# Performance work log

Measured on AMD Instinct MI355X. Metric: run time of the kernel, lower is better.

The kernel has to match this reference:

```python
import jax, jax.numpy as jnp
import numpy as np

D_MODEL = 1024
NUM_HEADS = 16
D_K = D_MODEL // NUM_HEADS


def setup_inputs() -> dict:
    key = jax.random.key(0)
    ks = jax.random.split(key, 11)
    B, S = 2, 2048
    s = 1.0 / np.sqrt(D_MODEL)
    return {
        "q": jax.random.normal(ks[0], (B, S, D_MODEL), jnp.float32),
        "k": jax.random.normal(ks[1], (B, S, D_MODEL), jnp.float32),
        "v": jax.random.normal(ks[2], (B, S, D_MODEL), jnp.float32),
        "w_q": jax.random.normal(ks[3], (D_MODEL, D_MODEL), jnp.float32) * s,
        "b_q": jnp.zeros((D_MODEL,), jnp.float32),
        "w_k": jax.random.normal(ks[4], (D_MODEL, D_MODEL), jnp.float32) * s,
        "b_k": jnp.zeros((D_MODEL,), jnp.float32),
        "w_v": jax.random.normal(ks[5], (D_MODEL, D_MODEL), jnp.float32) * s,
        "b_v": jnp.zeros((D_MODEL,), jnp.float32),
        "w_o": jax.random.normal(ks[6], (D_MODEL, D_MODEL), jnp.float32) * s,
        "b_o": jnp.zeros((D_MODEL,), jnp.float32),
    }


def reference(q, k, v, w_q, b_q, w_k, b_k, w_v, b_v, w_o, b_o):
    B, S, _ = q.shape
    H, Dk = NUM_HEADS, D_K

    def split_heads(x):  # [B,S,D] -> [B,H,S,Dk]
        return x.reshape(B, S, H, Dk).transpose(0, 2, 1, 3)

    # torch nn.Linear: x @ W.T + b
    qh = split_heads(q @ w_q.T + b_q)
    kh = split_heads(k @ w_k.T + b_k)
    vh = split_heads(v @ w_v.T + b_v)

    scale = 1.0 / jnp.sqrt(jnp.asarray(Dk, qh.dtype))
    scores = jnp.einsum("bhsd,bhtd->bhst", qh, kh) * scale  # [B,H,S,S]
    attn = jax.nn.softmax(scores, axis=-1)
    # dropout is identity in eval/deterministic baseline
    out = jnp.einsum("bhst,bhtd->bhsd", attn, vh)  # [B,H,S,Dk]
    out = out.transpose(0, 2, 1, 3).reshape(B, S, H * Dk)
    return out @ w_o.T + b_o
```

## Files before the change

### kernel.cpp

```cpp
#include <hip/hip_runtime.h>
#include <hip/hip_bf16.h>
#include <stdint.h>

typedef unsigned short u16;
typedef __attribute__((ext_vector_type(8))) short short8;
typedef __attribute__((ext_vector_type(8))) __bf16 bf16x8;
typedef __attribute__((ext_vector_type(4))) float f32x4;
typedef __attribute__((ext_vector_type(4))) uint32_t u32x4;

#if defined(__has_builtin)
#if __has_builtin(__builtin_amdgcn_global_load_lds)
#define USE_GLLDS 1
#endif
#endif

#if defined(__has_builtin)
#if __has_builtin(__builtin_amdgcn_exp2f)
#define HAVE_EXP2_BUILTIN 1
#endif
#endif
__device__ __forceinline__ float fexp2(float x) {
#ifdef HAVE_EXP2_BUILTIN
  return __builtin_amdgcn_exp2f(x);
#else
  return exp2f(x);
#endif
}

__device__ __forceinline__ u16 f2bf(float f) {
  __hip_bfloat16 h = __float2bfloat16(f);
  return __builtin_bit_cast(u16, h);
}

__device__ __forceinline__ uint32_t cvt_pk_bf16(float lo, float hi) {
  uint32_t w;
  asm("v_cvt_pk_bf16_f32 %0, %1, %2" : "=v"(w) : "v"(lo), "v"(hi));
  return w;
}

__device__ __forceinline__ f32x4 mfma16(bf16x8 a, bf16x8 b, f32x4 c) {
  return __builtin_amdgcn_mfma_f32_16x16x32_bf16(a, b, c, 0, 0, 0);
}

#ifdef USE_GLLDS
__device__ __forceinline__ void async_cp16(const void* g, void* l) {
  __builtin_amdgcn_global_load_lds(
      (const __attribute__((address_space(1))) void*)g,
      (__attribute__((address_space(3))) void*)l, 16, 0, 0);
}
#endif

__global__ __launch_bounds__(256) void cvt_all(
    const float* __restrict__ q, const float* __restrict__ k,
    const float* __restrict__ v, const float* __restrict__ w0,
    const float* __restrict__ w1, const float* __restrict__ w2,
    const float* __restrict__ w3, u16* __restrict__ dst) {
  size_t i = ((size_t)blockIdx.x * 256 + threadIdx.x) * 8;
  const size_t M1 = 1u << 20;
  const float* s;
  size_t base;
  if (i < 4 * M1) { s = q; base = 0; }
  else if (i < 8 * M1) { s = k; base = 4 * M1; }
  else if (i < 12 * M1) { s = v; base = 8 * M1; }
  else if (i < 13 * M1) { s = w0; base = 12 * M1; }
  else if (i < 14 * M1) { s = w1; base = 13 * M1; }
  else if (i < 15 * M1) { s = w2; base = 14 * M1; }
  else { s = w3; base = 15 * M1; }
  const float4 a = *(const float4*)(s + (i - base));
  const float4 b = *(const float4*)(s + (i - base) + 4);
  short8 r;
  r[0] = (short)f2bf(a.x); r[1] = (short)f2bf(a.y);
  r[2] = (short)f2bf(a.z); r[3] = (short)f2bf(a.w);
  r[4] = (short)f2bf(b.x); r[5] = (short)f2bf(b.y);
  r[6] = (short)f2bf(b.z); r[7] = (short)f2bf(b.w);
  *(short8*)(dst + i) = r;
}

__device__ __forceinline__ void gemm_core8(const u16* __restrict__ X,
                                           const u16* __restrict__ W,
                                           const float* __restrict__ bias,
                                           void* __restrict__ outp, int mode,
                                           int m0, int n0) {
  __shared__ u16 Al[128 * 64];
  __shared__ u16 Bl[128 * 64];
  const int tid = threadIdx.x;
  const int wv = tid >> 6, l = tid & 63;
  const int wr = wv >> 2, wc = wv & 3;
  const int lrow = l & 15, g = l >> 4;
  const int rswe = (lrow & 7) << 3;

  f32x4 acc[4][2];
#pragma unroll
  for (int i = 0; i < 4; ++i)
#pragma unroll
    for (int j = 0; j < 2; ++j) acc[i][j] = (f32x4){0.f, 0.f, 0.f, 0.f};

  const int srow = l >> 3;
  const int gcol = ((l & 7) ^ srow) * 8;
  const u16* Asrc = X + (size_t)(m0 + wv * 8 + srow) * 1024 + gcol;
  const u16* Bsrc = W + (size_t)(wv * 8 + srow) * 1024 + gcol;

  for (int kt = 0; kt < 1024; kt += 64) {
#ifdef USE_GLLDS
    async_cp16(Asrc + kt, &Al[(wv * 8) * 64]);
    async_cp16(Asrc + (size_t)64 * 1024 + kt, &Al[(wv * 8 + 64) * 64]);
    async_cp16(Bsrc + kt, &Bl[(wv * 8) * 64]);
    async_cp16(Bsrc + (size_t)64 * 1024 + kt, &Bl[(wv * 8 + 64) * 64]);
#else
    short8 a0 = *(const short8*)(Asrc + kt);
    short8 a1 = *(const short8*)(Asrc + (size_t)64 * 1024 + kt);
    short8 b0 = *(const short8*)(Bsrc + kt);
    short8 b1 = *(const short8*)(Bsrc + (size_t)64 * 1024 + kt);
    *(short8*)&Al[(wv * 8 + srow) * 64 + (l & 7) * 8] = a0;
    *(short8*)&Al[(wv * 8 + 64 + srow) * 64 + (l & 7) * 8] = a1;
    *(short8*)&Bl[(wv * 8 + srow) * 64 + (l & 7) * 8] = b0;
    *(short8*)&Bl[(wv * 8 + 64 + srow) * 64 + (l & 7) * 8] = b1;
#endif
    __syncthreads();
#pragma unroll
    for (int ks = 0; ks < 2; ++ks) {
      bf16x8 af[4], bf[2];
      const int qoff = (((ks * 4 + g) << 3) ^ rswe);
#pragma unroll
      for (int mf = 0; mf < 4; ++mf)
        af[mf] = *(const bf16x8*)&Al[(wr * 64 + mf * 16 + lrow) * 64 + qoff];
#pragma unroll
      for (int nf = 0; nf < 2; ++nf)
        bf[nf] = *(const bf16x8*)&Bl[(wc * 32 + nf * 16 + lrow) * 64 + qoff];
#pragma unroll
      for (int mf = 0; mf < 4; ++mf)
#pragma unroll
        for (int nf = 0; nf < 2; ++nf)
          acc[mf][nf] = mfma16(af[mf], bf[nf], acc[mf][nf]);
    }
    __syncthreads();
  }

  const int rb = (l >> 4) * 4;
#pragma unroll
  for (int mf = 0; mf < 4; ++mf) {
#pragma unroll
    for (int nf = 0; nf < 2; ++nf) {
      const int gn = n0 + wc * 32 + nf * 16 + lrow;
      const float bi = bias[gn];
#pragma unroll
      for (int r = 0; r < 4; ++r) {
        const int gm = m0 + wr * 64 + mf * 16 + rb + r;
        float val = acc[mf][nf][r] + bi;
        const int b = gm >> 11, s = gm & 2047, h = gn >> 6, d = gn & 63;
        if (mode == 3) {
          ((float*)outp)[(size_t)gm * 1024 + gn] = val;
        } else if (mode == 2) {
          ((u16*)outp)[(((size_t)((b * 16 + h) * 64 + d)) << 11) + s] = f2bf(val);
        } else {
          if (mode == 0) val *= 0.18033688f;
          ((u16*)outp)[(((size_t)((b * 16 + h) * 2048 + s)) << 6) + d] = f2bf(val);
        }
      }
    }
  }
}

__global__ __launch_bounds__(512, 6) void gemm_proj(
    const u16* __restrict__ qb, const u16* __restrict__ wqb,
    const float* __restrict__ b_q, const float* __restrict__ b_k,
    const float* __restrict__ b_v, u16* __restrict__ Qh) {
  const int s = blockIdx.x;
  const int xcd = s & 7, c = s >> 3;
  const int nx = (xcd >> 2) * 12 + (c % 12);
  const int my = (xcd & 3) * 8 + (c / 12);
  const int z = nx >> 3, nxl = nx & 7;
  const float* bias = (z == 0) ? b_q : ((z == 1) ? b_k : b_v);
  gemm_core8(qb + ((size_t)z << 22), wqb + ((size_t)nx << 17), bias,
             Qh + ((size_t)z << 22), z, my * 128, nxl * 128);
}

__global__ __launch_bounds__(512, 6) void gemm_out(
    const u16* __restrict__ X, const u16* __restrict__ W,
    const float* __restrict__ bias, float* __restrict__ out) {
  const int s = blockIdx.x;
  const int xcd = s & 7, c = s >> 3;
  const int nx = (xcd >> 2) * 4 + (c & 3);
  const int my = (xcd & 3) * 8 + (c >> 2);
  gemm_core8(X, W + ((size_t)nx << 17), bias, out, 3, my * 128, nx * 128);
}

__global__ __launch_bounds__(512, 4) void flash_attn7(
    const u16* __restrict__ Qh, const u16* __restrict__ Kh,
    const u16* __restrict__ VT, u16* __restrict__ Op,
    float2* __restrict__ ml) {
  __shared__ __align__(16) u16 Kbuf[2][4096];
  __shared__ __align__(16) u16 Vbuf[2][4096];
  __shared__ __align__(16) uint32_t Pl[8 * 576];

  const int tid = threadIdx.x;
  const int wv = tid >> 6, l = tid & 63;
  const int q = l & 15, g = l >> 4;

  const int s_lin = blockIdx.x + (blockIdx.y << 4) + (blockIdx.z << 9);
  const int o = ((s_lin & 7) << 7) + (s_lin >> 3);
  const int qt = o & 15, bh = (o >> 4) & 31, z = o >> 9;

  const u16* Qp = Qh + ((size_t)bh * 2048 + qt * 128 + wv * 16) * 64;
  const u16* Kp = Kh + (size_t)bh * 2048 * 64;
  const u16* Vp = VT + (size_t)bh * 64 * 2048;

  bf16x8 qf[2];
  qf[0] = *(const bf16x8*)(Qp + q * 64 + g * 8);
  qf[1] = *(const bf16x8*)(Qp + q * 64 + 32 + g * 8);

  f32x4 o_acc[4];
#pragma unroll
  for (int df = 0; df < 4; ++df) o_acc[df] = (f32x4){0.f, 0.f, 0.f, 0.f};
  float m = -1e30f, ls = 0.f;

  const int srow = l >> 3;
  const int scolq = (l & 7) ^ srow;
  const int pbase = wv * 576 + q * 36;
  const char* kb0 = (const char*)&Kbuf[0][0];
  const char* kb1 = (const char*)&Kbuf[1][0];
  const char* vb0 = (const char*)&Vbuf[0][0];
  const char* vb1 = (const char*)&Vbuf[1][0];
  const int rsw = (q & 7) << 4;

  const u16* kg = Kp + (size_t)(z * 1024 + wv * 8 + srow) * 64 + scolq * 8;
  const u16* vg = Vp + (size_t)(wv * 8 + srow) * 2048 + z * 1024 + scolq * 8;

  {
    short8 k0 = *(const short8*)kg;
    short8 k1 = *(const short8*)(kg + 4096);
    short8 v0 = *(const short8*)vg;
    short8 v1 = *(const short8*)(vg + 64);
    *(short8*)&Kbuf[0][wv * 512 + l * 8] = k0;
    *(short8*)&Kbuf[1][wv * 512 + l * 8] = k1;
    *(short8*)&Vbuf[0][wv * 512 + l * 8] = v0;
    *(short8*)&Vbuf[1][wv * 512 + l * 8] = v1;
  }
  kg += 8192;
  vg += 128;
  __syncthreads();

  for (int tt = 0; tt < 8; ++tt) {
    short8 kr0, kr1, vr0, vr1;
    if (tt < 7) {
      kr0 = *(const short8*)kg;
      kr1 = *(const short8*)(kg + 4096);
      vr0 = *(const short8*)vg;
      vr1 = *(const short8*)(vg + 64);
      kg += 8192;
      vg += 128;
    }

    f32x4 s0[4], s1[4];
#pragma unroll
    for (int nj = 0; nj < 4; ++nj) {
      s0[nj] = (f32x4){0.f, 0.f, 0.f, 0.f};
      s1[nj] = (f32x4){0.f, 0.f, 0.f, 0.f};
    }
#pragma unroll
    for (int ks = 0; ks < 2; ++ks) {
#pragma unroll
      for (int nj = 0; nj < 4; ++nj) {
        const int off = (nj * 16 + q) * 128 + (((ks * 4 + g) << 4) ^ rsw);
        bf16x8 kf0 = *(const bf16x8*)(kb0 + off);
        bf16x8 kf1 = *(const bf16x8*)(kb1 + off);
        s0[nj] = mfma16(kf0, qf[ks], s0[nj]);
        s1[nj] = mfma16(kf1, qf[ks], s1[nj]);
      }
    }

    float mt = s0[0][0];
#pragma unroll
    for (int nj = 0; nj < 4; ++nj)
#pragma unroll
      for (int r = 0; r < 4; ++r) {
        mt = fmaxf(mt, s0[nj][r]);
        mt = fmaxf(mt, s1[nj][r]);
      }
    mt = fmaxf(mt, __shfl_xor(mt, 16));
    mt = fmaxf(mt, __shfl_xor(mt, 32));
    if (!__all(mt <= m + 8.f)) {
      const float nm = fmaxf(m, mt);
      const float rf = fexp2(m - nm);
      m = nm;
      ls *= rf;
#pragma unroll
      for (int df = 0; df < 4; ++df) o_acc[df] *= rf;
    }
    float ps = 0.f;
#pragma unroll
    for (int nj = 0; nj < 4; ++nj)
#pragma unroll
      for (int r = 0; r < 4; ++r) {
        s0[nj][r] = fexp2(s0[nj][r] - m);
        s1[nj][r] = fexp2(s1[nj][r] - m);
        ps += s0[nj][r] + s1[nj][r];
      }
    ps += __shfl_xor(ps, 16);
    ps += __shfl_xor(ps, 32);
    ls += ps;

#pragma unroll
    for (int nj = 0; nj < 4; ++nj)
#pragma unroll
      for (int pp = 0; pp < 2; ++pp)
        Pl[pbase + nj * 8 + g * 2 + pp] =
            cvt_pk_bf16(s0[nj][2 * pp], s0[nj][2 * pp + 1]);
#pragma unroll
    for (int ks = 0; ks < 2; ++ks) {
      u32x4 pw = *(const u32x4*)&Pl[pbase + ks * 16 + 4 * g];
      bf16x8 pf = __builtin_bit_cast(bf16x8, pw);
#pragma unroll
      for (int df = 0; df < 4; ++df) {
        bf16x8 vf = *(const bf16x8*)(vb0 + (df * 16 + q) * 128 +
                                     (((ks * 4 + g) << 4) ^ rsw));
        o_acc[df] = mfma16(vf, pf, o_acc[df]);
      }
    }

#pragma unroll
    for (int nj = 0; nj < 4; ++nj)
#pragma unroll
      for (int pp = 0; pp < 2; ++pp)
        Pl[pbase + nj * 8 + g * 2 + pp] =
            cvt_pk_bf16(s1[nj][2 * pp], s1[nj][2 * pp + 1]);
#pragma unroll
    for (int ks = 0; ks < 2; ++ks) {
      u32x4 pw = *(const u32x4*)&Pl[pbase + ks * 16 + 4 * g];
      bf16x8 pf = __builtin_bit_cast(bf16x8, pw);
#pragma unroll
      for (int df = 0; df < 4; ++df) {
        bf16x8 vf = *(const bf16x8*)(vb1 + (df * 16 + q) * 128 +
                                     (((ks * 4 + g) << 4) ^ rsw));
        o_acc[df] = mfma16(vf, pf, o_acc[df]);
      }
    }

    __syncthreads();
    if (tt < 7) {
      *(short8*)&Kbuf[0][wv * 512 + l * 8] = kr0;
      *(short8*)&Kbuf[1][wv * 512 + l * 8] = kr1;
      *(short8*)&Vbuf[0][wv * 512 + l * 8] = vr0;
      *(short8*)&Vbuf[1][wv * 512 + l * 8] = vr1;
    }
    __syncthreads();
  }

  const float inv = 1.f / ls;
  const int rowb = qt * 128 + wv * 16 + q;
  const size_t prow = (size_t)(z * 32 + bh) * 2048 + rowb;
  u16* Po = Op + (prow << 6);
#pragma unroll
  for (int df = 0; df < 4; ++df)
#pragma unroll
    for (int pp = 0; pp < 2; ++pp) {
      uint32_t w = cvt_pk_bf16(o_acc[df][2 * pp] * inv,
                               o_acc[df][2 * pp + 1] * inv);
      *(uint32_t*)(Po + df * 16 + 4 * g + 2 * pp) = w;
    }
  if (g == 0) ml[prow] = make_float2(m, ls);
}

__global__ __launch_bounds__(256) void combine(
    const uint32_t* __restrict__ Op32, const float2* __restrict__ ml,
    u16* __restrict__ AO) {
  const int j = blockIdx.x * 256 + threadIdx.x;
  const int rowid = j >> 5, w5 = j & 31;
  const float2 a = ml[rowid];
  const float2 c = ml[(1 << 16) + rowid];
  const float M = fmaxf(a.x, c.x);
  float w1 = a.y * fexp2(a.x - M);
  float w2 = c.y * fexp2(c.x - M);
  const float inv = 1.f / (w1 + w2);
  w1 *= inv;
  w2 *= inv;
  const uint32_t p1 = Op32[j];
  const uint32_t p2 = Op32[(1u << 21) + j];
  const float lo = w1 * __builtin_bit_cast(float, p1 << 16) +
                   w2 * __builtin_bit_cast(float, p2 << 16);
  const float hi = w1 * __builtin_bit_cast(float, p1 & 0xffff0000u) +
                   w2 * __builtin_bit_cast(float, p2 & 0xffff0000u);
  const uint32_t outw = cvt_pk_bf16(lo, hi);
  const int bh = rowid >> 11, s = rowid & 2047, b = bh >> 4, h = bh & 15;
  ((uint32_t*)AO)[((size_t)(b * 2048 + s) << 9) + h * 32 + w5] = outw;
}

extern "C" void kernel_launch(void* const* d_in, const int* in_sizes, int n_in,
                              void* d_out, int out_size, void* d_ws,
                              size_t ws_size, hipStream_t stream) {
  const float* q = (const float*)d_in[0];
  const float* k = (const float*)d_in[1];
  const float* v = (const float*)d_in[2];
  const float* w_q = (const float*)d_in[3];
  const float* b_q = (const float*)d_in[4];
  const float* w_k = (const float*)d_in[5];
  const float* b_k = (const float*)d_in[6];
  const float* w_v = (const float*)d_in[7];
  const float* b_v = (const float*)d_in[8];
  const float* w_o = (const float*)d_in[9];
  const float* b_o = (const float*)d_in[10];

  u16* ws = (u16*)d_ws;
  u16* qb = ws;
  u16* wqb = ws + (12u << 20);
  u16* wob = ws + (15u << 20);
  u16* Qh = ws + (16u << 20);
  u16* Kh = ws + (20u << 20);
  u16* VT = ws + (24u << 20);
  u16* AO = ws + (28u << 20);
  u16* Op = ws;
  float2* ml = (float2*)(ws + (8u << 20));

  cvt_all<<<dim3(8192), dim3(256), 0, stream>>>(q, k, v, w_q, w_k, w_v, w_o, ws);
  gemm_proj<<<dim3(768), dim3(512), 0, stream>>>(qb, wqb, b_q, b_k, b_v, Qh);
  flash_attn7<<<dim3(16, 32, 2), dim3(512), 0, stream>>>(Qh, Kh, VT, Op, ml);
  combine<<<dim3(8192), dim3(256), 0, stream>>>((const uint32_t*)Op, ml, AO);
  gemm_out<<<dim3(256), dim3(512), 0, stream>>>(AO, wob, b_o, (float*)d_out);
}
```

Measured before the change: 144.6 us.

## Fuse fp32-to-bf16 conversion into GEMM loads and raise MFMA wave priority

Drops the standalone cvt_all kernel. The projection and output GEMMs now read fp32 activations and weights directly, converting them to bf16 in registers before staging into LDS. This removes one launch and the round trip of writing and re-reading the bf16 copies. In exchange, the GEMM loads become synchronous (no global_load_lds) and move twice as many bytes, and weights are converted again by every block that reads them. It also wraps the MFMA sections in the GEMMs and attention with s_setprio to favour waves issuing matrix ops.

```diff
diff --git a/kernel.cpp b/kernel.cpp
--- a/kernel.cpp
+++ b/kernel.cpp
@@ -38,6 +38,17 @@
   return w;
 }
 
+__device__ __forceinline__ short8 pack8_f32(const float* p) {
+  const float4 lo = *(const float4*)p;
+  const float4 hi = *(const float4*)(p + 4);
+  union { uint32_t u[4]; short8 s; } r;
+  r.u[0] = cvt_pk_bf16(lo.x, lo.y);
+  r.u[1] = cvt_pk_bf16(lo.z, lo.w);
+  r.u[2] = cvt_pk_bf16(hi.x, hi.y);
+  r.u[3] = cvt_pk_bf16(hi.z, hi.w);
+  return r.s;
+}
+
 __device__ __forceinline__ f32x4 mfma16(bf16x8 a, bf16x8 b, f32x4 c) {
   return __builtin_amdgcn_mfma_f32_16x16x32_bf16(a, b, c, 0, 0, 0);
 }
@@ -50,34 +61,9 @@
 }
 #endif
 
-__global__ __launch_bounds__(256) void cvt_all(
-    const float* __restrict__ q, const float* __restrict__ k,
-    const float* __restrict__ v, const float* __restrict__ w0,
-    const float* __restrict__ w1, const float* __restrict__ w2,
-    const float* __restrict__ w3, u16* __restrict__ dst) {
-  size_t i = ((size_t)blockIdx.x * 256 + threadIdx.x) * 8;
-  const size_t M1 = 1u << 20;
-  const float* s;
-  size_t base;
-  if (i < 4 * M1) { s = q; base = 0; }
-  else if (i < 8 * M1) { s = k; base = 4 * M1; }
-  else if (i < 12 * M1) { s = v; base = 8 * M1; }
-  else if (i < 13 * M1) { s = w0; base = 12 * M1; }
-  else if (i < 14 * M1) { s = w1; base = 13 * M1; }
-  else if (i < 15 * M1) { s = w2; base = 14 * M1; }
-  else { s = w3; base = 15 * M1; }
-  const float4 a = *(const float4*)(s + (i - base));
-  const float4 b = *(const float4*)(s + (i - base) + 4);
-  short8 r;
-  r[0] = (short)f2bf(a.x); r[1] = (short)f2bf(a.y);
-  r[2] = (short)f2bf(a.z); r[3] = (short)f2bf(a.w);
-  r[4] = (short)f2bf(b.x); r[5] = (short)f2bf(b.y);
-  r[6] = (short)f2bf(b.z); r[7] = (short)f2bf(b.w);
-  *(short8*)(dst + i) = r;
-}
-
-__device__ __forceinline__ void gemm_core8(const u16* __restrict__ X,
-                                           const u16* __restrict__ W,
+template <int A_F32, int B_F32>
+__device__ __forceinline__ void gemm_core8(const void* __restrict__ Xv,
+                                           const void* __restrict__ Wv,
                                            const float* __restrict__ bias,
                                            void* __restrict__ outp, int mode,
                                            int m0, int n0) {
@@ -96,26 +82,51 @@
     for (int j = 0; j < 2; ++j) acc[i][j] = (f32x4){0.f, 0.f, 0.f, 0.f};
 
   const int srow = l >> 3;
-  const int gcol = ((l & 7) ^ srow) * 8;
-  const u16* Asrc = X + (size_t)(m0 + wv * 8 + srow) * 1024 + gcol;
-  const u16* Bsrc = W + (size_t)(wv * 8 + srow) * 1024 + gcol;
+  const int ccol = l & 7;
+  const int gchunk = ccol ^ srow;
+  const int arow = wv * 8 + srow;
 
   for (int kt = 0; kt < 1024; kt += 64) {
+    if (A_F32) {
+      const float* Af = (const float*)Xv;
+      const float* pa = Af + (size_t)(m0 + arow) * 1024 + kt + gchunk * 8;
+      short8 a0 = pack8_f32(pa);
+      short8 a1 = pack8_f32(pa + (size_t)64 * 1024);
+      *(short8*)&Al[arow * 64 + ccol * 8] = a0;
+      *(short8*)&Al[(arow + 64) * 64 + ccol * 8] = a1;
+    } else {
+      const u16* Ab = (const u16*)Xv;
+      const u16* Asrc = Ab + (size_t)(m0 + arow) * 1024 + kt + gchunk * 8;
 #ifdef USE_GLLDS
-    async_cp16(Asrc + kt, &Al[(wv * 8) * 64]);
-    async_cp16(Asrc + (size_t)64 * 1024 + kt, &Al[(wv * 8 + 64) * 64]);
-    async_cp16(Bsrc + kt, &Bl[(wv * 8) * 64]);
-    async_cp16(Bsrc + (size_t)64 * 1024 + kt, &Bl[(wv * 8 + 64) * 64]);
+      async_cp16(Asrc, &Al[(wv * 8) * 64]);
+      async_cp16(Asrc + (size_t)64 * 1024, &Al[(wv * 8 + 64) * 64]);
 #else
-    short8 a0 = *(const short8*)(Asrc + kt);
-    short8 a1 = *(const short8*)(Asrc + (size_t)64 * 1024 + kt);
-    short8 b0 = *(const short8*)(Bsrc + kt);
-    short8 b1 = *(const short8*)(Bsrc + (size_t)64 * 1024 + kt);
-    *(short8*)&Al[(wv * 8 + srow) * 64 + (l & 7) * 8] = a0;
-    *(short8*)&Al[(wv * 8 + 64 + srow) * 64 + (l & 7) * 8] = a1;
-    *(short8*)&Bl[(wv * 8 + srow) * 64 + (l & 7) * 8] = b0;
-    *(short8*)&Bl[(wv * 8 + 64 + srow) * 64 + (l & 7) * 8] = b1;
-#endif
+      short8 a0 = *(const short8*)Asrc;
+      short8 a1 = *(const short8*)(Asrc + (size_t)64 * 1024);
+      *(short8*)&Al[arow * 64 + ccol * 8] = a0;
+      *(short8*)&Al[(arow + 64) * 64 + ccol * 8] = a1;
+#endif
+    }
+    if (B_F32) {
+      const float* Wf = (const float*)Wv;
+      const float* pb = Wf + (size_t)arow * 1024 + kt + gchunk * 8;
+      short8 b0 = pack8_f32(pb);
+      short8 b1 = pack8_f32(pb + (size_t)64 * 1024);
+      *(short8*)&Bl[arow * 64 + ccol * 8] = b0;
+      *(short8*)&Bl[(arow + 64) * 64 + ccol * 8] = b1;
+    } else {
+      const u16* Wb = (const u16*)Wv;
+      const u16* Bsrc = Wb + (size_t)arow * 1024 + kt + gchunk * 8;
+#ifdef USE_GLLDS
+      async_cp16(Bsrc, &Bl[(wv * 8) * 64]);
+      async_cp16(Bsrc + (size_t)64 * 1024, &Bl[(wv * 8 + 64) * 64]);
+#else
+      short8 b0 = *(const short8*)Bsrc;
+      short8 b1 = *(const short8*)(Bsrc + (size_t)64 * 1024);
+      *(short8*)&Bl[arow * 64 + ccol * 8] = b0;
+      *(short8*)&Bl[(arow + 64) * 64 + ccol * 8] = b1;
+#endif
+    }
     __syncthreads();
 #pragma unroll
     for (int ks = 0; ks < 2; ++ks) {
@@ -127,11 +138,13 @@
 #pragma unroll
       for (int nf = 0; nf < 2; ++nf)
         bf[nf] = *(const bf16x8*)&Bl[(wc * 32 + nf * 16 + lrow) * 64 + qoff];
+      __builtin_amdgcn_s_setprio(1);
 #pragma unroll
       for (int mf = 0; mf < 4; ++mf)
 #pragma unroll
         for (int nf = 0; nf < 2; ++nf)
           acc[mf][nf] = mfma16(af[mf], bf[nf], acc[mf][nf]);
+      __builtin_amdgcn_s_setprio(0);
     }
     __syncthreads();
   }
@@ -162,7 +175,9 @@
 }
 
 __global__ __launch_bounds__(512, 6) void gemm_proj(
-    const u16* __restrict__ qb, const u16* __restrict__ wqb,
+    const float* __restrict__ q, const float* __restrict__ k,
+    const float* __restrict__ v, const float* __restrict__ w_q,
+    const float* __restrict__ w_k, const float* __restrict__ w_v,
     const float* __restrict__ b_q, const float* __restrict__ b_k,
     const float* __restrict__ b_v, u16* __restrict__ Qh) {
   const int s = blockIdx.x;
@@ -170,22 +185,25 @@
   const int nx = (xcd >> 2) * 12 + (c % 12);
   const int my = (xcd & 3) * 8 + (c / 12);
   const int z = nx >> 3, nxl = nx & 7;
+  const float* X = (z == 0) ? q : ((z == 1) ? k : v);
+  const float* W = (z == 0) ? w_q : ((z == 1) ? w_k : w_v);
   const float* bias = (z == 0) ? b_q : ((z == 1) ? b_k : b_v);
-  gemm_core8(qb + ((size_t)z << 22), wqb + ((size_t)nx << 17), bias,
-             Qh + ((size_t)z << 22), z, my * 128, nxl * 128);
+  gemm_core8<1, 1>(X, W + ((size_t)nxl << 17), bias, Qh + ((size_t)z << 22),
+                   z, my * 128, nxl * 128);
 }
 
 __global__ __launch_bounds__(512, 6) void gemm_out(
-    const u16* __restrict__ X, const u16* __restrict__ W,
+    const u16* __restrict__ X, const float* __restrict__ W,
     const float* __restrict__ bias, float* __restrict__ out) {
   const int s = blockIdx.x;
   const int xcd = s & 7, c = s >> 3;
   const int nx = (xcd >> 2) * 4 + (c & 3);
   const int my = (xcd & 3) * 8 + (c >> 2);
-  gemm_core8(X, W + ((size_t)nx << 17), bias, out, 3, my * 128, nx * 128);
-}
-
-__global__ __launch_bounds__(512, 4) void flash_attn7(
+  gemm_core8<0, 1>(X, W + ((size_t)nx << 17), bias, out, 3, my * 128,
+                   nx * 128);
+}
+
+__global__ __launch_bounds__(512, 4) void flash_attn8(
     const u16* __restrict__ Qh, const u16* __restrict__ Kh,
     const u16* __restrict__ VT, u16* __restrict__ Op,
     float2* __restrict__ ml) {
@@ -257,6 +275,7 @@
       s0[nj] = (f32x4){0.f, 0.f, 0.f, 0.f};
       s1[nj] = (f32x4){0.f, 0.f, 0.f, 0.f};
     }
+    __builtin_amdgcn_s_setprio(1);
 #pragma unroll
     for (int ks = 0; ks < 2; ++ks) {
 #pragma unroll
@@ -268,6 +287,7 @@
         s1[nj] = mfma16(kf1, qf[ks], s1[nj]);
       }
     }
+    __builtin_amdgcn_s_setprio(0);
 
     float mt = s0[0][0];
 #pragma unroll
@@ -306,6 +326,7 @@
       for (int pp = 0; pp < 2; ++pp)
         Pl[pbase + nj * 8 + g * 2 + pp] =
             cvt_pk_bf16(s0[nj][2 * pp], s0[nj][2 * pp + 1]);
+    __builtin_amdgcn_s_setprio(1);
 #pragma unroll
     for (int ks = 0; ks < 2; ++ks) {
       u32x4 pw = *(const u32x4*)&Pl[pbase + ks * 16 + 4 * g];
@@ -317,6 +338,7 @@
         o_acc[df] = mfma16(vf, pf, o_acc[df]);
       }
     }
+    __builtin_amdgcn_s_setprio(0);
 
 #pragma unroll
     for (int nj = 0; nj < 4; ++nj)
@@ -324,6 +346,7 @@
       for (int pp = 0; pp < 2; ++pp)
         Pl[pbase + nj * 8 + g * 2 + pp] =
             cvt_pk_bf16(s1[nj][2 * pp], s1[nj][2 * pp + 1]);
+    __builtin_amdgcn_s_setprio(1);
 #pragma unroll
     for (int ks = 0; ks < 2; ++ks) {
       u32x4 pw = *(const u32x4*)&Pl[pbase + ks * 16 + 4 * g];
@@ -335,6 +358,7 @@
         o_acc[df] = mfma16(vf, pf, o_acc[df]);
       }
     }
+    __builtin_amdgcn_s_setprio(0);
 
     __syncthreads();
     if (tt < 7) {
@@ -401,9 +425,6 @@
   const float* b_o = (const float*)d_in[10];
 
   u16* ws = (u16*)d_ws;
-  u16* qb = ws;
-  u16* wqb = ws + (12u << 20);
-  u16* wob = ws + (15u << 20);
   u16* Qh = ws + (16u << 20);
   u16* Kh = ws + (20u << 20);
   u16* VT = ws + (24u << 20);
@@ -411,9 +432,9 @@
   u16* Op = ws;
   float2* ml = (float2*)(ws + (8u << 20));
 
-  cvt_all<<<dim3(8192), dim3(256), 0, stream>>>(q, k, v, w_q, w_k, w_v, w_o, ws);
-  gemm_proj<<<dim3(768), dim3(512), 0, stream>>>(qb, wqb, b_q, b_k, b_v, Qh);
-  flash_attn7<<<dim3(16, 32, 2), dim3(512), 0, stream>>>(Qh, Kh, VT, Op, ml);
+  gemm_proj<<<dim3(768), dim3(512), 0, stream>>>(q, k, v, w_q, w_k, w_v, b_q,
+                                                 b_k, b_v, Qh);
+  flash_attn8<<<dim3(16, 32, 2), dim3(512), 0, stream>>>(Qh, Kh, VT, Op, ml);
   combine<<<dim3(8192), dim3(256), 0, stream>>>((const uint32_t*)Op, ml, AO);
-  gemm_out<<<dim3(256), dim3(512), 0, stream>>>(AO, wob, b_o, (float*)d_out);
-}
+  gemm_out<<<dim3(256), dim3(512), 0, stream>>>(AO, w_o, b_o, (float*)d_out);
+}
```

Result: no change. 142.0 us (-1.8%).
